# Kernel optimization log

Hardware: AMD Instinct MI355X
Metric: run time of the kernel (lower is better)

The kernel has to match this reference:

```python
import jax, jax.numpy as jnp
import numpy as np

EMBED_DIM = 1024
NUM_HEADS = 16
HEAD_DIM = EMBED_DIM // NUM_HEADS


def setup_inputs() -> dict:
    key = jax.random.key(0)
    k1, k2, k3, k4, k5 = jax.random.split(key, 5)
    B, N, C = 4, 2048, EMBED_DIM
    s = 1.0 / np.sqrt(C)
    return {
        "x": jax.random.normal(k1, (B, N, C), dtype=jnp.float32),
        "w_qkv": jax.random.uniform(k2, (C, 3 * C), dtype=jnp.float32, minval=-s, maxval=s),
        "b_qkv": jax.random.uniform(k3, (3 * C,), dtype=jnp.float32, minval=-s, maxval=s),
        "w_out": jax.random.uniform(k4, (C, C), dtype=jnp.float32, minval=-s, maxval=s),
        "b_out": jax.random.uniform(k5, (C,), dtype=jnp.float32, minval=-s, maxval=s),
    }


def reference(x, w_qkv, b_qkv, w_out, b_out):
    B, N, C = x.shape
    H, D = NUM_HEADS, HEAD_DIM
    qkv = x @ w_qkv + b_qkv                       # [B, N, 3C]
    qkv = qkv.reshape(B, N, 3, H, D)
    q = qkv[:, :, 0].transpose(0, 2, 1, 3)        # [B, H, N, D]
    k = qkv[:, :, 1].transpose(0, 2, 1, 3)
    v = qkv[:, :, 2].transpose(0, 2, 1, 3)
    scale = 1.0 / np.sqrt(D).astype(np.float32)
    attn = jnp.einsum('bhnd,bhmd->bhnm', q, k) * scale  # [B, H, N, N]
    attn = jax.nn.softmax(attn, axis=-1)
    out = jnp.einsum('bhnm,bhmd->bhnd', attn, v)  # [B, H, N, D]
    out = out.transpose(0, 2, 1, 3).reshape(B, N, C)
    return out @ w_out + b_out
```

## Files before the change

### kernel.cpp

```cpp
#include <hip/hip_runtime.h>


typedef unsigned short u16;
typedef __bf16 bf16x8 __attribute__((ext_vector_type(8)));
typedef float f32x4 __attribute__((ext_vector_type(4)));

#define MFMA(a, b, c) __builtin_amdgcn_mfma_f32_16x16x32_bf16(a, b, c, 0, 0, 0)

__device__ __forceinline__ u16 f2bf(float f) {
    __bf16 h = (__bf16)f;
    return *(u16*)&h;
}

__device__ __forceinline__ void gld16(const void* g, void* l) {
    __builtin_amdgcn_global_load_lds(
        (const __attribute__((address_space(1))) void*)g,
        (__attribute__((address_space(3))) void*)l, 16, 0, 0);
}

__global__ __launch_bounds__(256) void cvt_f32_bf16(
    const float* __restrict__ src, u16* __restrict__ dst, long n)
{
    long i = ((long)blockIdx.x * 256 + threadIdx.x) * 8;
    if (i >= n) return;
    float4 a = *(const float4*)&src[i];
    float4 b = *(const float4*)&src[i + 4];
    union { u16 u[8]; uint4 v; } tmp;
    tmp.u[0] = f2bf(a.x); tmp.u[1] = f2bf(a.y);
    tmp.u[2] = f2bf(a.z); tmp.u[3] = f2bf(a.w);
    tmp.u[4] = f2bf(b.x); tmp.u[5] = f2bf(b.y);
    tmp.u[6] = f2bf(b.z); tmp.u[7] = f2bf(b.w);
    *(uint4*)&dst[i] = tmp.v;
}

__global__ __launch_bounds__(256) void transpose_f2b(
    const float* __restrict__ src, u16* __restrict__ dst, int R, int C)
{
    __shared__ alignas(16) u16 tile[64 * 80];
    const int r0 = blockIdx.y * 64, c0 = blockIdx.x * 64;
    const int t = threadIdx.x;
#pragma unroll
    for (int c = 0; c < 4; c++) {
        int idx = t + c * 256;
        int r = idx >> 4, seg = idx & 15;
        float4 f = *(const float4*)&src[(long)(r0 + r) * C + c0 + seg * 4];
        u16* p = &tile[r * 80 + seg * 4];
        p[0] = f2bf(f.x); p[1] = f2bf(f.y); p[2] = f2bf(f.z); p[3] = f2bf(f.w);
    }
    __syncthreads();
#pragma unroll
    for (int c = 0; c < 2; c++) {
        int idx = t + c * 256;
        int rr = idx >> 3, seg = idx & 7;
        union { u16 u[8]; uint4 v; } tmp;
#pragma unroll
        for (int j = 0; j < 8; j++) tmp.u[j] = tile[(seg * 8 + j) * 80 + rr];
        *(uint4*)&dst[(long)(c0 + rr) * R + r0 + seg * 8] = tmp.v;
    }
}

__global__ __launch_bounds__(256) void transpose64(
    const u16* __restrict__ src, u16* __restrict__ dst,
    int R, int C, long sstride, long dstride)
{
    __shared__ alignas(16) u16 tile[64 * 80];
    const u16* s = src + (long)blockIdx.z * sstride;
    u16* d = dst + (long)blockIdx.z * dstride;
    const int r0 = blockIdx.y * 64, c0 = blockIdx.x * 64;
    const int t = threadIdx.x;
#pragma unroll
    for (int c = 0; c < 2; c++) {
        int idx = t + c * 256;
        int r = idx >> 3, seg = idx & 7;
        *(uint4*)&tile[r * 80 + seg * 8] =
            *(const uint4*)&s[(long)(r0 + r) * C + c0 + seg * 8];
    }
    __syncthreads();
#pragma unroll
    for (int c = 0; c < 2; c++) {
        int idx = t + c * 256;
        int rr = idx >> 3, seg = idx & 7;
        union { u16 u[8]; uint4 v; } tmp;
#pragma unroll
        for (int j = 0; j < 8; j++) tmp.u[j] = tile[(seg * 8 + j) * 80 + rr];
        *(uint4*)&d[(long)(c0 + rr) * R + r0 + seg * 8] = tmp.v;
    }
}

template <int EPI>
__global__ __launch_bounds__(256) void gemm_bf16(
    const u16* __restrict__ A, const u16* __restrict__ Bt,
    const float* __restrict__ bias,
    u16* __restrict__ out0, u16* __restrict__ out1, u16* __restrict__ out2,
    float* __restrict__ outf,
    int M, int N, int K)
{
    const int m0 = blockIdx.x * 128, n0 = blockIdx.y * 128;
    const int t = threadIdx.x;
    const int wave = t >> 6, lane = t & 63, quad = lane >> 4, l15 = lane & 15;
    const int wm = wave >> 1, wn = wave & 1;

    __shared__ alignas(16) u16 As[128 * 32];
    __shared__ alignas(16) u16 Bs[128 * 32];

    const int srow = wave * 32 + (lane >> 2);
    const int scol = (lane & 3) * 8;

    f32x4 acc[4][4] = {};

    for (int k0 = 0; k0 < K; k0 += 32) {
        __syncthreads();
#pragma unroll
        for (int c = 0; c < 2; c++) {
            gld16(&A[(long)(m0 + srow + c * 16) * K + k0 + scol],
                  &As[(wave * 32 + c * 16) * 32]);
            gld16(&Bt[(long)(n0 + srow + c * 16) * K + k0 + scol],
                  &Bs[(wave * 32 + c * 16) * 32]);
        }
        __syncthreads();

        bf16x8 af[4], bf[4];
#pragma unroll
        for (int mt = 0; mt < 4; mt++)
            af[mt] = *(bf16x8*)&As[(wm * 64 + mt * 16 + l15) * 32 + quad * 8];
#pragma unroll
        for (int nt = 0; nt < 4; nt++)
            bf[nt] = *(bf16x8*)&Bs[(wn * 64 + nt * 16 + l15) * 32 + quad * 8];
#pragma unroll
        for (int mt = 0; mt < 4; mt++)
#pragma unroll
            for (int nt = 0; nt < 4; nt++)
                acc[mt][nt] = MFMA(af[mt], bf[nt], acc[mt][nt]);
    }

#pragma unroll
    for (int mt = 0; mt < 4; mt++) {
#pragma unroll
        for (int nt = 0; nt < 4; nt++) {
            int cg = n0 + wn * 64 + nt * 16 + l15;
            float bv = bias[cg];
            if (EPI == 0) {
                int t3 = cg >> 10;
                int hh = (cg >> 6) & 15, dd = cg & 63;
#pragma unroll
                for (int r = 0; r < 4; r++) {
                    int row = m0 + wm * 64 + mt * 16 + quad * 4 + r;
                    float val = acc[mt][nt][r] + bv;
                    int bb = row >> 11, nn = row & 2047;
                    long di = ((long)((bb << 4) + hh) * 2048 + nn) * 64 + dd;
                    if (t3 == 0)      out0[di] = f2bf(val * 0.125f);
                    else if (t3 == 1) out1[di] = f2bf(val);
                    else              out2[di] = f2bf(val);
                }
            } else {
#pragma unroll
                for (int r = 0; r < 4; r++) {
                    int row = m0 + wm * 64 + mt * 16 + quad * 4 + r;
                    outf[(long)row * N + cg] = acc[mt][nt][r] + bv;
                }
            }
        }
    }
}

__global__ __launch_bounds__(256, 4) void flash_attn(
    const u16* __restrict__ q, const u16* __restrict__ k,
    const u16* __restrict__ vt, u16* __restrict__ attn)
{
    const int bh = blockIdx.y;
    const int b = bh >> 4, h = bh & 15;
    const int q0 = blockIdx.x * 128;
    const int t = threadIdx.x;
    const int wave = t >> 6, lane = t & 63, quad = lane >> 4, l15 = lane & 15;

    __shared__ alignas(16) u16 Ks[64 * 72];
    __shared__ alignas(16) u16 Vs[64 * 72];
    __shared__ alignas(16) __bf16 Ps[128 * 72];

    bf16x8 qf[2][2];
#pragma unroll
    for (int mt = 0; mt < 2; mt++) {
        long row = (long)bh * 2048 + q0 + wave * 32 + mt * 16 + l15;
        qf[mt][0] = *(const bf16x8*)&q[row * 64 + quad * 8];
        qf[mt][1] = *(const bf16x8*)&q[row * 64 + 32 + quad * 8];
    }

    bf16x8 ones;
#pragma unroll
    for (int j = 0; j < 8; j++) ones[j] = (__bf16)1.0f;

    f32x4 o[2][4] = {};
    f32x4 ls[2] = {};

    for (int kt = 0; kt < 32; kt++) {
        __syncthreads();
#pragma unroll
        for (int c = 0; c < 2; c++) {
            int idx = t + c * 256;
            int r = idx >> 3, seg = idx & 7;
            *(uint4*)&Ks[r * 72 + seg * 8] =
                *(const uint4*)&k[((long)bh * 2048 + kt * 64 + r) * 64 + seg * 8];
            *(uint4*)&Vs[r * 72 + seg * 8] =
                *(const uint4*)&vt[((long)bh * 64 + r) * 2048 + kt * 64 + seg * 8];
        }
        __syncthreads();

#pragma unroll
        for (int mt = 0; mt < 2; mt++) {
            f32x4 s[4];
#pragma unroll
            for (int ct = 0; ct < 4; ct++) {
                bf16x8 kf0 = *(bf16x8*)&Ks[(ct * 16 + l15) * 72 + quad * 8];
                bf16x8 kf1 = *(bf16x8*)&Ks[(ct * 16 + l15) * 72 + 32 + quad * 8];
                f32x4 z = {};
                z = MFMA(qf[mt][0], kf0, z);
                s[ct] = MFMA(qf[mt][1], kf1, z);
            }
#pragma unroll
            for (int ct = 0; ct < 4; ct++)
#pragma unroll
                for (int r = 0; r < 4; r++)
                    Ps[(wave * 32 + mt * 16 + quad * 4 + r) * 72 + ct * 16 + l15] =
                        (__bf16)__expf(s[ct][r]);
        }
        __syncthreads();

#pragma unroll
        for (int mt = 0; mt < 2; mt++) {
            bf16x8 pa0 = *(bf16x8*)&Ps[(wave * 32 + mt * 16 + l15) * 72 + quad * 8];
            bf16x8 pa1 = *(bf16x8*)&Ps[(wave * 32 + mt * 16 + l15) * 72 + 32 + quad * 8];
            ls[mt] = MFMA(pa0, ones, ls[mt]);
            ls[mt] = MFMA(pa1, ones, ls[mt]);
#pragma unroll
            for (int dt = 0; dt < 4; dt++) {
                bf16x8 vb0 = *(bf16x8*)&Vs[(dt * 16 + l15) * 72 + quad * 8];
                bf16x8 vb1 = *(bf16x8*)&Vs[(dt * 16 + l15) * 72 + 32 + quad * 8];
                o[mt][dt] = MFMA(pa0, vb0, o[mt][dt]);
                o[mt][dt] = MFMA(pa1, vb1, o[mt][dt]);
            }
        }
    }

#pragma unroll
    for (int mt = 0; mt < 2; mt++) {
#pragma unroll
        for (int r = 0; r < 4; r++) {
            float inv = 1.f / ls[mt][r];
            int n = q0 + wave * 32 + mt * 16 + quad * 4 + r;
#pragma unroll
            for (int dt = 0; dt < 4; dt++) {
                attn[((long)b * 2048 + n) * 1024 + h * 64 + dt * 16 + l15] =
                    f2bf(o[mt][dt][r] * inv);
            }
        }
    }
}

extern "C" void kernel_launch(void* const* d_in, const int* in_sizes, int n_in,
                              void* d_out, int out_size, void* d_ws, size_t ws_size,
                              hipStream_t stream) {
    const float* x     = (const float*)d_in[0];
    const float* w_qkv = (const float*)d_in[1];
    const float* b_qkv = (const float*)d_in[2];
    const float* w_out = (const float*)d_in[3];
    const float* b_out = (const float*)d_in[4];
    float* out = (float*)d_out;

    u16* ws    = (u16*)d_ws;
    u16* q     = ws;
    u16* kk    = q + 8388608;
    u16* v     = kk + 8388608;
    u16* vt    = v + 8388608;
    u16* attn  = vt + 8388608;
    u16* x_bf  = attn + 8388608;
    u16* wqkvT = x_bf + 8388608;
    u16* woutT = wqkvT + 3145728;

    cvt_f32_bf16<<<4096, 256, 0, stream>>>(x, x_bf, 8388608L);
    transpose_f2b<<<dim3(48, 16), 256, 0, stream>>>(w_qkv, wqkvT, 1024, 3072);
    transpose_f2b<<<dim3(16, 16), 256, 0, stream>>>(w_out, woutT, 1024, 1024);
    gemm_bf16<0><<<dim3(64, 24), 256, 0, stream>>>(x_bf, wqkvT, b_qkv, q, kk, v,
                                                   nullptr, 8192, 3072, 1024);
    transpose64<<<dim3(1, 32, 64), 256, 0, stream>>>(v, vt, 2048, 64,
                                                     2048L * 64, 64L * 2048);
    flash_attn<<<dim3(16, 64), 256, 0, stream>>>(q, kk, vt, attn);
    gemm_bf16<1><<<dim3(64, 8), 256, 0, stream>>>(attn, woutT, b_out, nullptr,
                                                  nullptr, nullptr, out,
                                                  8192, 1024, 1024);
}
```

Baseline: 311.6 us.

## Fuse V transpose into QKV GEMM epilogue and drop LDS staging in attention

The QKV GEMM now swaps the MFMA operands so each lane holds four consecutive output columns. This allows packed 8-byte stores for Q and K, and V is written directly in transposed layout, so the separate transpose kernel is removed. The attention kernel no longer stages K and V tiles through shared memory. It reads MFMA fragments straight from global memory with swapped operands, which removes two barriers per tile and also packs the P writes and output stores. The cost is uncoalesced 2-byte strided stores for V^T and repeated global (cache) reads of K/V by each wave instead of shared LDS reuse.

```diff
diff --git a/kernel.cpp b/kernel.cpp
--- a/kernel.cpp
+++ b/kernel.cpp
@@ -2,6 +2,7 @@
 
 
 typedef unsigned short u16;
+typedef unsigned long long u64;
 typedef __bf16 bf16x8 __attribute__((ext_vector_type(8)));
 typedef float f32x4 __attribute__((ext_vector_type(4)));
 
@@ -59,34 +60,6 @@
     }
 }
 
-__global__ __launch_bounds__(256) void transpose64(
-    const u16* __restrict__ src, u16* __restrict__ dst,
-    int R, int C, long sstride, long dstride)
-{
-    __shared__ alignas(16) u16 tile[64 * 80];
-    const u16* s = src + (long)blockIdx.z * sstride;
-    u16* d = dst + (long)blockIdx.z * dstride;
-    const int r0 = blockIdx.y * 64, c0 = blockIdx.x * 64;
-    const int t = threadIdx.x;
-#pragma unroll
-    for (int c = 0; c < 2; c++) {
-        int idx = t + c * 256;
-        int r = idx >> 3, seg = idx & 7;
-        *(uint4*)&tile[r * 80 + seg * 8] =
-            *(const uint4*)&s[(long)(r0 + r) * C + c0 + seg * 8];
-    }
-    __syncthreads();
-#pragma unroll
-    for (int c = 0; c < 2; c++) {
-        int idx = t + c * 256;
-        int rr = idx >> 3, seg = idx & 7;
-        union { u16 u[8]; uint4 v; } tmp;
-#pragma unroll
-        for (int j = 0; j < 8; j++) tmp.u[j] = tile[(seg * 8 + j) * 80 + rr];
-        *(uint4*)&d[(long)(c0 + rr) * R + r0 + seg * 8] = tmp.v;
-    }
-}
-
 template <int EPI>
 __global__ __launch_bounds__(256) void gemm_bf16(
     const u16* __restrict__ A, const u16* __restrict__ Bt,
@@ -130,34 +103,45 @@
         for (int mt = 0; mt < 4; mt++)
 #pragma unroll
             for (int nt = 0; nt < 4; nt++)
-                acc[mt][nt] = MFMA(af[mt], bf[nt], acc[mt][nt]);
+                acc[mt][nt] = MFMA(bf[nt], af[mt], acc[mt][nt]);
     }
 
 #pragma unroll
     for (int mt = 0; mt < 4; mt++) {
+        int token = m0 + wm * 64 + mt * 16 + l15;
+        int bb = token >> 11, nn = token & 2047;
 #pragma unroll
         for (int nt = 0; nt < 4; nt++) {
-            int cg = n0 + wn * 64 + nt * 16 + l15;
-            float bv = bias[cg];
+            int cgb = n0 + wn * 64 + nt * 16 + quad * 4;
+            float4 bv = *(const float4*)&bias[cgb];
+            float v0 = acc[mt][nt][0] + bv.x;
+            float v1 = acc[mt][nt][1] + bv.y;
+            float v2 = acc[mt][nt][2] + bv.z;
+            float v3 = acc[mt][nt][3] + bv.w;
             if (EPI == 0) {
-                int t3 = cg >> 10;
-                int hh = (cg >> 6) & 15, dd = cg & 63;
-#pragma unroll
-                for (int r = 0; r < 4; r++) {
-                    int row = m0 + wm * 64 + mt * 16 + quad * 4 + r;
-                    float val = acc[mt][nt][r] + bv;
-                    int bb = row >> 11, nn = row & 2047;
-                    long di = ((long)((bb << 4) + hh) * 2048 + nn) * 64 + dd;
-                    if (t3 == 0)      out0[di] = f2bf(val * 0.125f);
-                    else if (t3 == 1) out1[di] = f2bf(val);
-                    else              out2[di] = f2bf(val);
+                int t3 = cgb >> 10;
+                int hh = (cgb >> 6) & 15, dd = cgb & 63;
+                int bh = (bb << 4) + hh;
+                if (t3 == 0) {
+                    union { u16 u[4]; u64 v; } pk;
+                    pk.u[0] = f2bf(v0 * 0.125f); pk.u[1] = f2bf(v1 * 0.125f);
+                    pk.u[2] = f2bf(v2 * 0.125f); pk.u[3] = f2bf(v3 * 0.125f);
+                    *(u64*)&out0[((long)bh * 2048 + nn) * 64 + dd] = pk.v;
+                } else if (t3 == 1) {
+                    union { u16 u[4]; u64 v; } pk;
+                    pk.u[0] = f2bf(v0); pk.u[1] = f2bf(v1);
+                    pk.u[2] = f2bf(v2); pk.u[3] = f2bf(v3);
+                    *(u64*)&out1[((long)bh * 2048 + nn) * 64 + dd] = pk.v;
+                } else {
+                    long vb = ((long)bh * 64 + dd) * 2048 + nn;
+                    out2[vb]            = f2bf(v0);
+                    out2[vb + 2048]     = f2bf(v1);
+                    out2[vb + 2 * 2048] = f2bf(v2);
+                    out2[vb + 3 * 2048] = f2bf(v3);
                 }
             } else {
-#pragma unroll
-                for (int r = 0; r < 4; r++) {
-                    int row = m0 + wm * 64 + mt * 16 + quad * 4 + r;
-                    outf[(long)row * N + cg] = acc[mt][nt][r] + bv;
-                }
+                float4 o4 = { v0, v1, v2, v3 };
+                *(float4*)&outf[(long)token * N + cgb] = o4;
             }
         }
     }
@@ -173,8 +157,6 @@
     const int t = threadIdx.x;
     const int wave = t >> 6, lane = t & 63, quad = lane >> 4, l15 = lane & 15;
 
-    __shared__ alignas(16) u16 Ks[64 * 72];
-    __shared__ alignas(16) u16 Vs[64 * 72];
     __shared__ alignas(16) __bf16 Ps[128 * 72];
 
     bf16x8 qf[2][2];
@@ -189,69 +171,73 @@
 #pragma unroll
     for (int j = 0; j < 8; j++) ones[j] = (__bf16)1.0f;
 
+    const u16* kb = k + (long)bh * 2048 * 64;
+    const u16* vb = vt + (long)bh * 64 * 2048;
+    const int prow = (wave * 32 + l15) * 72;
+
     f32x4 o[2][4] = {};
     f32x4 ls[2] = {};
 
     for (int kt = 0; kt < 32; kt++) {
-        __syncthreads();
-#pragma unroll
-        for (int c = 0; c < 2; c++) {
-            int idx = t + c * 256;
-            int r = idx >> 3, seg = idx & 7;
-            *(uint4*)&Ks[r * 72 + seg * 8] =
-                *(const uint4*)&k[((long)bh * 2048 + kt * 64 + r) * 64 + seg * 8];
-            *(uint4*)&Vs[r * 72 + seg * 8] =
-                *(const uint4*)&vt[((long)bh * 64 + r) * 2048 + kt * 64 + seg * 8];
-        }
-        __syncthreads();
-
+        f32x4 st[2][4];
+#pragma unroll
+        for (int ct = 0; ct < 4; ct++) {
+            const u16* kr = kb + (kt * 64 + ct * 16 + l15) * 64;
+            bf16x8 kf0 = *(const bf16x8*)&kr[quad * 8];
+            bf16x8 kf1 = *(const bf16x8*)&kr[32 + quad * 8];
+#pragma unroll
+            for (int mt = 0; mt < 2; mt++) {
+                f32x4 z = {};
+                z = MFMA(kf0, qf[mt][0], z);
+                st[mt][ct] = MFMA(kf1, qf[mt][1], z);
+            }
+        }
+
+        __syncthreads();
+#pragma unroll
+        for (int mt = 0; mt < 2; mt++)
+#pragma unroll
+            for (int ct = 0; ct < 4; ct++) {
+                union { u16 u[4]; u64 v; } pk;
+#pragma unroll
+                for (int r = 0; r < 4; r++)
+                    pk.u[r] = f2bf(__expf(st[mt][ct][r]));
+                *(u64*)&Ps[prow + mt * 16 * 72 + ct * 16 + quad * 4] = pk.v;
+            }
+        __syncthreads();
+
+        bf16x8 pb[2][2];
 #pragma unroll
         for (int mt = 0; mt < 2; mt++) {
-            f32x4 s[4];
-#pragma unroll
-            for (int ct = 0; ct < 4; ct++) {
-                bf16x8 kf0 = *(bf16x8*)&Ks[(ct * 16 + l15) * 72 + quad * 8];
-                bf16x8 kf1 = *(bf16x8*)&Ks[(ct * 16 + l15) * 72 + 32 + quad * 8];
-                f32x4 z = {};
-                z = MFMA(qf[mt][0], kf0, z);
-                s[ct] = MFMA(qf[mt][1], kf1, z);
-            }
-#pragma unroll
-            for (int ct = 0; ct < 4; ct++)
-#pragma unroll
-                for (int r = 0; r < 4; r++)
-                    Ps[(wave * 32 + mt * 16 + quad * 4 + r) * 72 + ct * 16 + l15] =
-                        (__bf16)__expf(s[ct][r]);
-        }
-        __syncthreads();
-
-#pragma unroll
-        for (int mt = 0; mt < 2; mt++) {
-            bf16x8 pa0 = *(bf16x8*)&Ps[(wave * 32 + mt * 16 + l15) * 72 + quad * 8];
-            bf16x8 pa1 = *(bf16x8*)&Ps[(wave * 32 + mt * 16 + l15) * 72 + 32 + quad * 8];
-            ls[mt] = MFMA(pa0, ones, ls[mt]);
-            ls[mt] = MFMA(pa1, ones, ls[mt]);
-#pragma unroll
-            for (int dt = 0; dt < 4; dt++) {
-                bf16x8 vb0 = *(bf16x8*)&Vs[(dt * 16 + l15) * 72 + quad * 8];
-                bf16x8 vb1 = *(bf16x8*)&Vs[(dt * 16 + l15) * 72 + 32 + quad * 8];
-                o[mt][dt] = MFMA(pa0, vb0, o[mt][dt]);
-                o[mt][dt] = MFMA(pa1, vb1, o[mt][dt]);
+            pb[mt][0] = *(bf16x8*)&Ps[prow + mt * 16 * 72 + quad * 8];
+            pb[mt][1] = *(bf16x8*)&Ps[prow + mt * 16 * 72 + 32 + quad * 8];
+            ls[mt] = MFMA(ones, pb[mt][0], ls[mt]);
+            ls[mt] = MFMA(ones, pb[mt][1], ls[mt]);
+        }
+#pragma unroll
+        for (int dt = 0; dt < 4; dt++) {
+            const u16* vr = vb + (dt * 16 + l15) * 2048 + kt * 64;
+            bf16x8 va0 = *(const bf16x8*)&vr[quad * 8];
+            bf16x8 va1 = *(const bf16x8*)&vr[32 + quad * 8];
+#pragma unroll
+            for (int mt = 0; mt < 2; mt++) {
+                o[mt][dt] = MFMA(va0, pb[mt][0], o[mt][dt]);
+                o[mt][dt] = MFMA(va1, pb[mt][1], o[mt][dt]);
             }
         }
     }
 
 #pragma unroll
     for (int mt = 0; mt < 2; mt++) {
-#pragma unroll
-        for (int r = 0; r < 4; r++) {
-            float inv = 1.f / ls[mt][r];
-            int n = q0 + wave * 32 + mt * 16 + quad * 4 + r;
-#pragma unroll
-            for (int dt = 0; dt < 4; dt++) {
-                attn[((long)b * 2048 + n) * 1024 + h * 64 + dt * 16 + l15] =
-                    f2bf(o[mt][dt][r] * inv);
-            }
+        float inv = 1.f / ls[mt][0];
+        int n = q0 + wave * 32 + mt * 16 + l15;
+#pragma unroll
+        for (int dt = 0; dt < 4; dt++) {
+            union { u16 u[4]; u64 v; } pk;
+#pragma unroll
+            for (int r = 0; r < 4; r++) pk.u[r] = f2bf(o[mt][dt][r] * inv);
+            *(u64*)&attn[((long)b * 2048 + n) * 1024 + h * 64 + dt * 16 + quad * 4] =
+                pk.v;
         }
     }
 }
@@ -269,8 +255,7 @@
     u16* ws    = (u16*)d_ws;
     u16* q     = ws;
     u16* kk    = q + 8388608;
-    u16* v     = kk + 8388608;
-    u16* vt    = v + 8388608;
+    u16* vt    = kk + 8388608;
     u16* attn  = vt + 8388608;
     u16* x_bf  = attn + 8388608;
     u16* wqkvT = x_bf + 8388608;
@@ -279,10 +264,8 @@
     cvt_f32_bf16<<<4096, 256, 0, stream>>>(x, x_bf, 8388608L);
     transpose_f2b<<<dim3(48, 16), 256, 0, stream>>>(w_qkv, wqkvT, 1024, 3072);
     transpose_f2b<<<dim3(16, 16), 256, 0, stream>>>(w_out, woutT, 1024, 1024);
-    gemm_bf16<0><<<dim3(64, 24), 256, 0, stream>>>(x_bf, wqkvT, b_qkv, q, kk, v,
+    gemm_bf16<0><<<dim3(64, 24), 256, 0, stream>>>(x_bf, wqkvT, b_qkv, q, kk, vt,
                                                    nullptr, 8192, 3072, 1024);
-    transpose64<<<dim3(1, 32, 64), 256, 0, stream>>>(v, vt, 2048, 64,
-                                                     2048L * 64, 64L * 2048);
     flash_attn<<<dim3(16, 64), 256, 0, stream>>>(q, kk, vt, attn);
     gemm_bf16<1><<<dim3(64, 8), 256, 0, stream>>>(attn, woutT, b_out, nullptr,
                                                   nullptr, nullptr, out,
```

Measured after the change: 430.2 us. 1.38x slower.
